# Performance work log

Hardware: AMD Instinct MI355X
Metric: run time of the kernel (lower is better)

The kernel has to match this reference:

```python
import jax, jax.numpy as jnp
import numpy as np

N = 50000        # nodes
E = 1_600_000    # edges (avg degree 32)
D_IN = 128
HID = 256
D_OUT = 128      # must equal D_IN for the residual add


def setup_inputs() -> dict:
    key = jax.random.key(0)
    k0, k1, k2, k3 = jax.random.split(key, 4)
    x = jax.random.normal(k0, (N, D_IN), dtype=jnp.float32)
    edge_index = jax.random.randint(k1, (2, E), 0, N, dtype=jnp.int32)
    # GCNConv params (lin: Linear without bias in PyG, plus additive bias)
    W1 = jax.random.normal(k2, (D_IN, HID), dtype=jnp.float32) / np.sqrt(D_IN)
    b1 = jnp.zeros((HID,), jnp.float32)
    W2 = jax.random.normal(k3, (HID, D_OUT), dtype=jnp.float32) / np.sqrt(HID)
    b2 = jnp.zeros((D_OUT,), jnp.float32)
    return {"x": x, "edge_index": edge_index, "W1": W1, "b1": b1, "W2": W2, "b2": b2}


def _gcn_conv(x, src, dst, norm, W, b, n):
    # PyG GCNConv: transform, gather source features, scale by sym-norm, scatter-add to dst.
    h = x @ W                        # [n, d_out]
    msg = h[src] * norm[:, None]     # [E+n, d_out] gathered messages
    out = jax.ops.segment_sum(msg, dst, num_segments=n)
    return out + b


def reference(x, edge_index, W1, b1, W2, b2):
    n = x.shape[0]
    # add self loops (GCNConv default add_self_loops=True)
    loops = jnp.arange(n, dtype=edge_index.dtype)
    src = jnp.concatenate([edge_index[0], loops])
    dst = jnp.concatenate([edge_index[1], loops])
    # symmetric normalization D^{-1/2} (A+I) D^{-1/2}
    deg = jax.ops.segment_sum(jnp.ones_like(dst, dtype=x.dtype), dst, num_segments=n)
    dinv = jnp.where(deg > 0, jax.lax.rsqrt(deg), 0.0)
    norm = dinv[src] * dinv[dst]
    skip = x  # nn.Identity skip connection
    h = jax.nn.relu(_gcn_conv(x, src, dst, norm, W1, b1, n))
    out = _gcn_conv(h, src, dst, norm, W2, b2, n)
    # classification_layer treated as identity; original .double() cast kept in fp32
    return out + skip
```

## Files before the change

kernel.cpp:

```cpp
#include <hip/hip_runtime.h>

#define D_IN 128
#define HID 256
#define BKT_SHIFT 8
#define BKT_SIZE 256
#define BKT_CAP 10240
#define CHUNK 4096
#define PAD_SLACK 2048
#define LSTR 264
#define ASTR 136

typedef __attribute__((ext_vector_type(8))) short short8;
typedef __attribute__((ext_vector_type(4))) float floatx4;
typedef __attribute__((ext_vector_type(4))) int intx4;

static __device__ __forceinline__ unsigned short f2b(float f) {
  unsigned u = __float_as_uint(f);
  unsigned r = (u + 0x7fffu + ((u >> 16) & 1u)) >> 16;
  return (unsigned short)r;
}

static __device__ __forceinline__ void unpack8(uint4 v, float* f) {
  f[0] = __uint_as_float(v.x << 16); f[1] = __uint_as_float(v.x & 0xffff0000u);
  f[2] = __uint_as_float(v.y << 16); f[3] = __uint_as_float(v.y & 0xffff0000u);
  f[4] = __uint_as_float(v.z << 16); f[5] = __uint_as_float(v.z & 0xffff0000u);
  f[6] = __uint_as_float(v.w << 16); f[7] = __uint_as_float(v.w & 0xffff0000u);
}

static __device__ __forceinline__ void acc_fma(float* acc, uint4 v, float w) {
  float g[8];
  unpack8(v, g);
#pragma unroll
  for (int d = 0; d < 8; ++d) acc[d] = fmaf(g[d], w, acc[d]);
}

static __device__ __forceinline__ void gather_row(float* acc, const uint4* __restrict__ Hq,
                                                  const float* __restrict__ dinv,
                                                  const int* __restrict__ csr,
                                                  int2 se, float dv, int lane) {
  intx4 c0 = *(const intx4*)(csr + se.x);
  intx4 c1 = *(const intx4*)(csr + se.x + 4);
  for (int j = se.x; j < se.y; ) {
    const int jn = j + 8;
    const int jp = (jn < se.y) ? jn : se.x;
    intx4 n0 = *(const intx4*)(csr + jp);
    intx4 n1 = *(const intx4*)(csr + jp + 4);
    float w0 = dinv[c0.x] * dv, w1 = dinv[c0.y] * dv;
    float w2 = dinv[c0.z] * dv, w3 = dinv[c0.w] * dv;
    float w4 = dinv[c1.x] * dv, w5 = dinv[c1.y] * dv;
    float w6 = dinv[c1.z] * dv, w7 = dinv[c1.w] * dv;
    uint4 v0 = Hq[(size_t)c0.x * 16 + lane];
    uint4 v1 = Hq[(size_t)c0.y * 16 + lane];
    uint4 v2 = Hq[(size_t)c0.z * 16 + lane];
    uint4 v3 = Hq[(size_t)c0.w * 16 + lane];
    uint4 v4 = Hq[(size_t)c1.x * 16 + lane];
    uint4 v5 = Hq[(size_t)c1.y * 16 + lane];
    uint4 v6 = Hq[(size_t)c1.z * 16 + lane];
    uint4 v7 = Hq[(size_t)c1.w * 16 + lane];
    acc_fma(acc, v0, w0);
    acc_fma(acc, v1, w1);
    acc_fma(acc, v2, w2);
    acc_fma(acc, v3, w3);
    acc_fma(acc, v4, w4);
    acc_fma(acc, v5, w5);
    acc_fma(acc, v6, w6);
    acc_fma(acc, v7, w7);
    c0 = n0; c1 = n1; j = jn;
  }
}


__global__ __launch_bounds__(256) void fused_front_kernel(
    const int* __restrict__ src, const int* __restrict__ dst,
    int* __restrict__ bkt_cursor, int* __restrict__ ebuf, int E, int nbkt, int nchunk,
    const float4* __restrict__ x4, unsigned short* __restrict__ xb, int n4,
    const float* __restrict__ W1, unsigned short* __restrict__ Wt1,
    const float* __restrict__ W2, unsigned short* __restrict__ Wt2,
    float* __restrict__ dinv, unsigned short* __restrict__ tb, int N) {
  const int bid = blockIdx.x;
  const int tid = threadIdx.x;
  if (bid < nchunk) {
    __shared__ int hist[BKT_SIZE];
    __shared__ int bbase[BKT_SIZE];
    if (tid < nbkt) hist[tid] = 0;
    __syncthreads();
    const int base = bid * CHUNK;
    const int end = min(base + CHUNK, E);
    for (int e = base + tid; e < end; e += 256)
      atomicAdd(&hist[dst[e] >> BKT_SHIFT], 1);
    __syncthreads();
    if (tid < nbkt) {
      int c = hist[tid];
      bbase[tid] = c > 0 ? atomicAdd(&bkt_cursor[tid], c) : 0;
      hist[tid] = 0;
    }
    __syncthreads();
    for (int e = base + tid; e < end; e += 256) {
      int d = dst[e];
      int b = d >> BKT_SHIFT;
      int off = atomicAdd(&hist[b], 1);
      int rel = bbase[b] + off;
      if (rel < BKT_CAP)
        ebuf[b * BKT_CAP + rel] = (src[e] << BKT_SHIFT) | (d & (BKT_SIZE - 1));
    }
    return;
  }
  const int nxblk = (n4 + 255) / 256;
  if (bid < nchunk + nxblk) {
    int i = (bid - nchunk) * 256 + tid;
    if (i >= n4) return;
    float4 v = x4[i];
    ushort4 o;
    o.x = f2b(v.x); o.y = f2b(v.y); o.z = f2b(v.z); o.w = f2b(v.w);
    *(ushort4*)(xb + (size_t)i * 4) = o;
  } else if (bid < nchunk + nxblk + 128) {
    int e = (bid - nchunk - nxblk) * 256 + tid;
    int k = e >> 8, n = e & 255;
    Wt1[(size_t)n * D_IN + k] = f2b(W1[e]);
  } else if (bid < nchunk + nxblk + 256) {
    int e = (bid - nchunk - nxblk - 128) * 256 + tid;
    int k = e >> 7, n = e & 127;
    Wt2[(size_t)n * HID + k] = f2b(W2[e]);
  } else {
    if (tid == 0) dinv[N] = 0.f;
    if (tid < 64)       ((unsigned*)(xb + (size_t)N * D_IN))[tid]      = 0u;
    else if (tid < 128) ((unsigned*)(tb + (size_t)N * D_IN))[tid - 64] = 0u;
  }
}


__global__ __launch_bounds__(256) void bucket_build_kernel(const int* __restrict__ ebuf,
                                                           const int* __restrict__ bkt_cursor,
                                                           float* __restrict__ dinv,
                                                           int2* __restrict__ rowse,
                                                           int* __restrict__ csr,
                                                           int N, int nbkt) {
  __shared__ int hist[BKT_SIZE];
  __shared__ int srs[BKT_SIZE];
  __shared__ int wsums[4];
  const int b = blockIdx.x;
  const int tid = threadIdx.x;
  const int node0 = b << BKT_SHIFT;
  const int nloc = min(BKT_SIZE, N - node0);
  const int ebeg = b * BKT_CAP;
  const int eend = ebeg + min(bkt_cursor[b], BKT_CAP);

  hist[tid] = 0;
  __syncthreads();
  for (int e = ebeg + tid; e < eend; e += 256)
    atomicAdd(&hist[ebuf[e] & (BKT_SIZE - 1)], 1);
  __syncthreads();

  const int h = hist[tid];
  const int p = (h + 7) & ~7;
  const int lane = tid & 63, wid = tid >> 6;
  int incl = p;
#pragma unroll
  for (int off = 1; off < 64; off <<= 1) {
    int t = __shfl_up(incl, off);
    if (lane >= off) incl += t;
  }
  if (lane == 63) wsums[wid] = incl;
  __syncthreads();
  int wex = 0;
  for (int w = 0; w < wid; ++w) wex += wsums[w];
  const int ex = wex + incl - p;
  const int base = b * (BKT_CAP + PAD_SLACK);
  if (tid < nloc) {
    int st = base + ex;
    dinv[node0 + tid] = rsqrtf((float)(h + 1));
    rowse[node0 + tid] = make_int2(st, st + p);
    srs[tid] = st;
  }
  hist[tid] = 0;
  __syncthreads();

  for (int e = ebeg + tid; e < eend; e += 256) {
    int u = ebuf[e];
    int l = u & (BKT_SIZE - 1);
    int pos = atomicAdd(&hist[l], 1);
    csr[srs[l] + pos] = u >> BKT_SHIFT;
  }
  __syncthreads();
  for (int l = tid; l < nloc; l += 256) {
    int deg = hist[l];
    int pp = (deg + 7) & ~7;
    int s0 = srs[l];
    for (int q = s0 + deg; q < s0 + pp; ++q) csr[q] = N;
  }
}


__global__ __launch_bounds__(512, 4) void agg1_gemm_kernel(
    const uint4* __restrict__ Hq, const int2* __restrict__ rowse,
    const int* __restrict__ csr, const float* __restrict__ dinv,
    const unsigned short* __restrict__ Wt1, const float* __restrict__ b1,
    const unsigned short* __restrict__ Wt2, unsigned short* __restrict__ T, int M) {
  __shared__ unsigned short as_[32][ASTR];
  __shared__ unsigned short hs[32][LSTR];
  const int tid = threadIdx.x;
  const int node0 = blockIdx.x * 32;

  {
    const int glane = tid & 15;
    const int lrow = tid >> 4;
    const int node = node0 + lrow;
    float acc[8] = {0.f, 0.f, 0.f, 0.f, 0.f, 0.f, 0.f, 0.f};
    if (node < M) {
      const float dv = dinv[node];
      uint4 sv = Hq[(size_t)node * 16 + glane];
      float f[8];
      unpack8(sv, f);
      const float ws = dv * dv;
#pragma unroll
      for (int d = 0; d < 8; ++d) acc[d] = f[d] * ws;
      gather_row(acc, Hq, dinv, csr, rowse[node], dv, glane);
    }
    uint4 o;
    o.x = (unsigned)f2b(acc[0]) | ((unsigned)f2b(acc[1]) << 16);
    o.y = (unsigned)f2b(acc[2]) | ((unsigned)f2b(acc[3]) << 16);
    o.z = (unsigned)f2b(acc[4]) | ((unsigned)f2b(acc[5]) << 16);
    o.w = (unsigned)f2b(acc[6]) | ((unsigned)f2b(acc[7]) << 16);
    *(uint4*)&as_[lrow][glane * 8] = o;
  }
  __syncthreads();

  const int wave = tid >> 6;
  const int lane = tid & 63;
  const int quad = lane >> 4;
  const int l16 = lane & 15;

  const short8* bp1 = (const short8*)(Wt1 + (size_t)(wave * 32 + l16) * D_IN + quad * 8);
  floatx4 acc1[2][2];
#pragma unroll
  for (int g = 0; g < 2; ++g)
#pragma unroll
    for (int t = 0; t < 2; ++t) acc1[g][t] = floatx4{0.f, 0.f, 0.f, 0.f};

#pragma unroll
  for (int kt = 0; kt < 4; ++kt) {
    short8 a0 = *(const short8*)&as_[0 * 16 + l16][kt * 32 + quad * 8];
    short8 a1 = *(const short8*)&as_[1 * 16 + l16][kt * 32 + quad * 8];
#pragma unroll
    for (int t = 0; t < 2; ++t) {
      short8 b = bp1[kt * 4 + t * 256];
      acc1[0][t] = __builtin_amdgcn_mfma_f32_16x16x32_bf16(a0, b, acc1[0][t], 0, 0, 0);
      acc1[1][t] = __builtin_amdgcn_mfma_f32_16x16x32_bf16(a1, b, acc1[1][t], 0, 0, 0);
    }
  }
#pragma unroll
  for (int t = 0; t < 2; ++t) {
    const float bv = b1[wave * 32 + t * 16 + l16];
#pragma unroll
    for (int g = 0; g < 2; ++g)
#pragma unroll
      for (int r = 0; r < 4; ++r) {
        float v = acc1[g][t][r] + bv;
        v = v > 0.f ? v : 0.f;
        hs[g * 16 + quad * 4 + r][wave * 32 + t * 16 + l16] = f2b(v);
      }
  }
  __syncthreads();

  const short8* bp2 = (const short8*)(Wt2 + (size_t)(wave * 16 + l16) * HID + quad * 8);
  floatx4 acc2[2];
#pragma unroll
  for (int g = 0; g < 2; ++g) acc2[g] = floatx4{0.f, 0.f, 0.f, 0.f};

#pragma unroll
  for (int kt = 0; kt < 8; ++kt) {
    short8 a0 = *(const short8*)&hs[0 * 16 + l16][kt * 32 + quad * 8];
    short8 a1 = *(const short8*)&hs[1 * 16 + l16][kt * 32 + quad * 8];
    short8 b = bp2[kt * 4];
    acc2[0] = __builtin_amdgcn_mfma_f32_16x16x32_bf16(a0, b, acc2[0], 0, 0, 0);
    acc2[1] = __builtin_amdgcn_mfma_f32_16x16x32_bf16(a1, b, acc2[1], 0, 0, 0);
  }
  __syncthreads();

#pragma unroll
  for (int g = 0; g < 2; ++g)
#pragma unroll
    for (int r = 0; r < 4; ++r)
      hs[g * 16 + quad * 4 + r][wave * 16 + l16] = f2b(acc2[g][r]);
  __syncthreads();

  {
    const int r = tid >> 4;
    const int c = (tid & 15) * 8;
    const int row = node0 + r;
    uint4 v = *(const uint4*)&hs[r][c];
    if (row < M) *(uint4*)&T[(size_t)row * D_IN + c] = v;
  }
}


__global__ __launch_bounds__(256) void agg2_kernel(const uint4* __restrict__ Hq,
                                                   const int2* __restrict__ rowse,
                                                   const int* __restrict__ csr,
                                                   const float* __restrict__ dinv,
                                                   const float* __restrict__ skip,
                                                   const float* __restrict__ bias,
                                                   float* __restrict__ OUT, int n) {
  const int lane = threadIdx.x & 15;
  const int node = blockIdx.x * 16 + (threadIdx.x >> 4);
  if (node >= n) return;

  const float dv = dinv[node];
  float acc[8];
  {
    uint4 sv = Hq[(size_t)node * 16 + lane];
    float f[8];
    unpack8(sv, f);
    const float ws = dv * dv;
#pragma unroll
    for (int d = 0; d < 8; ++d) acc[d] = f[d] * ws;
  }
  gather_row(acc, Hq, dinv, csr, rowse[node], dv, lane);

  const float* sp = skip + (size_t)node * 128 + lane * 8;
  const float* bp = bias + lane * 8;
  float4 s0 = *(const float4*)sp, s1 = *(const float4*)(sp + 4);
  float4 b0 = *(const float4*)bp, b1 = *(const float4*)(bp + 4);
  float* op = OUT + (size_t)node * 128 + lane * 8;
  *(float4*)op = make_float4(acc[0] + s0.x + b0.x, acc[1] + s0.y + b0.y,
                             acc[2] + s0.z + b0.z, acc[3] + s0.w + b0.w);
  *(float4*)(op + 4) = make_float4(acc[4] + s1.x + b1.x, acc[5] + s1.y + b1.y,
                                   acc[6] + s1.z + b1.z, acc[7] + s1.w + b1.w);
}


extern "C" void kernel_launch(void* const* d_in, const int* in_sizes, int n_in,
                              void* d_out, int out_size, void* d_ws, size_t ws_size,
                              hipStream_t stream) {
  const float* x  = (const float*)d_in[0];
  const int*   ei = (const int*)d_in[1];
  const float* W1 = (const float*)d_in[2];
  const float* b1 = (const float*)d_in[3];
  const float* W2 = (const float*)d_in[4];
  const float* b2 = (const float*)d_in[5];
  float* out = (float*)d_out;

  const int N = in_sizes[0] / D_IN;
  const int E = in_sizes[1] / 2;
  const int* srcA = ei;
  const int* dstA = ei + E;
  const int NBKT = (N + BKT_SIZE - 1) >> BKT_SHIFT;
  const int NCHUNK = (E + CHUNK - 1) / CHUNK;

  char* ws = (char*)d_ws;
  size_t off = 0;
  auto alloc = [&](size_t bytes) { void* p = ws + off; off = (off + bytes + 255) & ~(size_t)255; return p; };
  int*            bkt_cursor = (int*)           alloc((size_t)NBKT * 4);
  float*          dinv       = (float*)         alloc((size_t)(N + 1) * 4);
  int2*           rowse      = (int2*)          alloc((size_t)N * 8);
  int*            ebuf       = (int*)           alloc((size_t)NBKT * BKT_CAP * 4);
  int*            csr        = (int*)           alloc((size_t)NBKT * (BKT_CAP + PAD_SLACK) * 4);
  unsigned short* xb         = (unsigned short*)alloc((size_t)(N + 1) * D_IN * 2);
  unsigned short* tb         = (unsigned short*)alloc((size_t)(N + 1) * D_IN * 2);
  unsigned short* Wt1        = (unsigned short*)alloc((size_t)D_IN * HID * 2);
  unsigned short* Wt2        = (unsigned short*)alloc((size_t)D_IN * HID * 2);

  const int n4 = N * D_IN / 4;
  const int nxblk = (n4 + 255) / 256;

  (void)hipMemsetAsync(bkt_cursor, 0, (size_t)NBKT * 4, stream);
  fused_front_kernel<<<NCHUNK + nxblk + 256 + 1, 256, 0, stream>>>(
      srcA, dstA, bkt_cursor, ebuf, E, NBKT, NCHUNK,
      (const float4*)x, xb, n4, W1, Wt1, W2, Wt2, dinv, tb, N);
  bucket_build_kernel<<<NBKT, 256, 0, stream>>>(ebuf, bkt_cursor, dinv, rowse, csr, N, NBKT);
  agg1_gemm_kernel<<<(N + 31) / 32, 512, 0, stream>>>((const uint4*)xb, rowse, csr, dinv,
                                                      Wt1, b1, Wt2, tb, N);
  agg2_kernel<<<(N + 15) / 16, 256, 0, stream>>>((const uint4*)tb, rowse, csr,
                                                 dinv, x, b2, out, N);
}
```

Measured before the change: 265.9 us.

## Merge all stages into one persistent cooperative kernel with grid syncs

Replaces the memset plus four separate kernel launches with a single cooperative persistent kernel. It uses grid-stride loops over virtual blocks and grid-wide syncs between the phases: bucketing, bf16 conversion, CSR build, aggregation+GEMM and final aggregation. The aim is to remove launch overhead and inter-kernel gaps. In exchange, the grid is capped by occupancy at 512 threads, the later phases lose the extra parallelism of the old larger launches, and the grid barriers add their own cost.

```diff
diff --git a/kernel.cpp b/kernel.cpp
--- a/kernel.cpp
+++ b/kernel.cpp
@@ -1,4 +1,5 @@
 #include <hip/hip_runtime.h>
+#include <hip/hip_cooperative_groups.h>
 
 #define D_IN 128
 #define HID 256
@@ -70,262 +71,250 @@
 }
 
 
-__global__ __launch_bounds__(256) void fused_front_kernel(
+__global__ __launch_bounds__(512) void mega_kernel(
     const int* __restrict__ src, const int* __restrict__ dst,
-    int* __restrict__ bkt_cursor, int* __restrict__ ebuf, int E, int nbkt, int nchunk,
-    const float4* __restrict__ x4, unsigned short* __restrict__ xb, int n4,
+    int* __restrict__ bkt_cursor, int* __restrict__ ebuf,
+    const float4* __restrict__ x4, unsigned short* __restrict__ xb,
     const float* __restrict__ W1, unsigned short* __restrict__ Wt1,
     const float* __restrict__ W2, unsigned short* __restrict__ Wt2,
-    float* __restrict__ dinv, unsigned short* __restrict__ tb, int N) {
-  const int bid = blockIdx.x;
-  const int tid = threadIdx.x;
-  if (bid < nchunk) {
-    __shared__ int hist[BKT_SIZE];
-    __shared__ int bbase[BKT_SIZE];
-    if (tid < nbkt) hist[tid] = 0;
-    __syncthreads();
-    const int base = bid * CHUNK;
+    float* __restrict__ dinv, int2* __restrict__ rowse, int* __restrict__ csr,
+    const float* __restrict__ b1v, unsigned short* __restrict__ tb,
+    const float* __restrict__ xskip, const float* __restrict__ b2v,
+    float* __restrict__ out,
+    int E, int N, int nbkt, int nchunk, int n4) {
+  namespace cg = cooperative_groups;
+  cg::grid_group gg = cg::this_grid();
+
+  __shared__ union {
+    struct { int hist[BKT_SIZE]; int bbase[BKT_SIZE]; } p1;
+    struct { int hist[BKT_SIZE]; int srs[BKT_SIZE]; int wsums[4]; } p2;
+    struct { unsigned short a[32][ASTR]; unsigned short h[32][LSTR]; } p3;
+  } sm;
+
+  const int bid = blockIdx.x, tid = threadIdx.x;
+  const int gdim = gridDim.x;
+  const int gtid = bid * 512 + tid;
+  const int gstr = gdim * 512;
+
+  for (int i = gtid; i < nbkt; i += gstr) bkt_cursor[i] = 0;
+  gg.sync();
+
+  for (int vb = bid; vb < nchunk; vb += gdim) {
+    if (tid < nbkt) sm.p1.hist[tid] = 0;
+    __syncthreads();
+    const int base = vb * CHUNK;
     const int end = min(base + CHUNK, E);
-    for (int e = base + tid; e < end; e += 256)
-      atomicAdd(&hist[dst[e] >> BKT_SHIFT], 1);
+    for (int e = base + tid; e < end; e += 512)
+      atomicAdd(&sm.p1.hist[dst[e] >> BKT_SHIFT], 1);
     __syncthreads();
     if (tid < nbkt) {
-      int c = hist[tid];
-      bbase[tid] = c > 0 ? atomicAdd(&bkt_cursor[tid], c) : 0;
-      hist[tid] = 0;
-    }
-    __syncthreads();
-    for (int e = base + tid; e < end; e += 256) {
+      int c = sm.p1.hist[tid];
+      sm.p1.bbase[tid] = c > 0 ? atomicAdd(&bkt_cursor[tid], c) : 0;
+      sm.p1.hist[tid] = 0;
+    }
+    __syncthreads();
+    for (int e = base + tid; e < end; e += 512) {
       int d = dst[e];
       int b = d >> BKT_SHIFT;
-      int off = atomicAdd(&hist[b], 1);
-      int rel = bbase[b] + off;
+      int off = atomicAdd(&sm.p1.hist[b], 1);
+      int rel = sm.p1.bbase[b] + off;
       if (rel < BKT_CAP)
         ebuf[b * BKT_CAP + rel] = (src[e] << BKT_SHIFT) | (d & (BKT_SIZE - 1));
     }
-    return;
-  }
-  const int nxblk = (n4 + 255) / 256;
-  if (bid < nchunk + nxblk) {
-    int i = (bid - nchunk) * 256 + tid;
-    if (i >= n4) return;
+    __syncthreads();
+  }
+  for (int i = gtid; i < n4; i += gstr) {
     float4 v = x4[i];
     ushort4 o;
     o.x = f2b(v.x); o.y = f2b(v.y); o.z = f2b(v.z); o.w = f2b(v.w);
     *(ushort4*)(xb + (size_t)i * 4) = o;
-  } else if (bid < nchunk + nxblk + 128) {
-    int e = (bid - nchunk - nxblk) * 256 + tid;
-    int k = e >> 8, n = e & 255;
-    Wt1[(size_t)n * D_IN + k] = f2b(W1[e]);
-  } else if (bid < nchunk + nxblk + 256) {
-    int e = (bid - nchunk - nxblk - 128) * 256 + tid;
-    int k = e >> 7, n = e & 127;
-    Wt2[(size_t)n * HID + k] = f2b(W2[e]);
-  } else {
-    if (tid == 0) dinv[N] = 0.f;
-    if (tid < 64)       ((unsigned*)(xb + (size_t)N * D_IN))[tid]      = 0u;
-    else if (tid < 128) ((unsigned*)(tb + (size_t)N * D_IN))[tid - 64] = 0u;
-  }
-}
-
-
-__global__ __launch_bounds__(256) void bucket_build_kernel(const int* __restrict__ ebuf,
-                                                           const int* __restrict__ bkt_cursor,
-                                                           float* __restrict__ dinv,
-                                                           int2* __restrict__ rowse,
-                                                           int* __restrict__ csr,
-                                                           int N, int nbkt) {
-  __shared__ int hist[BKT_SIZE];
-  __shared__ int srs[BKT_SIZE];
-  __shared__ int wsums[4];
-  const int b = blockIdx.x;
-  const int tid = threadIdx.x;
-  const int node0 = b << BKT_SHIFT;
-  const int nloc = min(BKT_SIZE, N - node0);
-  const int ebeg = b * BKT_CAP;
-  const int eend = ebeg + min(bkt_cursor[b], BKT_CAP);
-
-  hist[tid] = 0;
-  __syncthreads();
-  for (int e = ebeg + tid; e < eend; e += 256)
-    atomicAdd(&hist[ebuf[e] & (BKT_SIZE - 1)], 1);
-  __syncthreads();
-
-  const int h = hist[tid];
-  const int p = (h + 7) & ~7;
-  const int lane = tid & 63, wid = tid >> 6;
-  int incl = p;
-#pragma unroll
-  for (int off = 1; off < 64; off <<= 1) {
-    int t = __shfl_up(incl, off);
-    if (lane >= off) incl += t;
-  }
-  if (lane == 63) wsums[wid] = incl;
-  __syncthreads();
-  int wex = 0;
-  for (int w = 0; w < wid; ++w) wex += wsums[w];
-  const int ex = wex + incl - p;
-  const int base = b * (BKT_CAP + PAD_SLACK);
-  if (tid < nloc) {
-    int st = base + ex;
-    dinv[node0 + tid] = rsqrtf((float)(h + 1));
-    rowse[node0 + tid] = make_int2(st, st + p);
-    srs[tid] = st;
-  }
-  hist[tid] = 0;
-  __syncthreads();
-
-  for (int e = ebeg + tid; e < eend; e += 256) {
-    int u = ebuf[e];
-    int l = u & (BKT_SIZE - 1);
-    int pos = atomicAdd(&hist[l], 1);
-    csr[srs[l] + pos] = u >> BKT_SHIFT;
-  }
-  __syncthreads();
-  for (int l = tid; l < nloc; l += 256) {
-    int deg = hist[l];
-    int pp = (deg + 7) & ~7;
-    int s0 = srs[l];
-    for (int q = s0 + deg; q < s0 + pp; ++q) csr[q] = N;
-  }
-}
-
-
-__global__ __launch_bounds__(512, 4) void agg1_gemm_kernel(
-    const uint4* __restrict__ Hq, const int2* __restrict__ rowse,
-    const int* __restrict__ csr, const float* __restrict__ dinv,
-    const unsigned short* __restrict__ Wt1, const float* __restrict__ b1,
-    const unsigned short* __restrict__ Wt2, unsigned short* __restrict__ T, int M) {
-  __shared__ unsigned short as_[32][ASTR];
-  __shared__ unsigned short hs[32][LSTR];
-  const int tid = threadIdx.x;
-  const int node0 = blockIdx.x * 32;
+  }
+  for (int e = gtid; e < D_IN * HID; e += gstr)
+    Wt1[(size_t)(e & 255) * D_IN + (e >> 8)] = f2b(W1[e]);
+  for (int e = gtid; e < HID * D_IN; e += gstr)
+    Wt2[(size_t)(e & 127) * HID + (e >> 7)] = f2b(W2[e]);
+  if (gtid == 0) dinv[N] = 0.f;
+  if (gtid < 64)       ((unsigned*)(xb + (size_t)N * D_IN))[gtid]      = 0u;
+  else if (gtid < 128) ((unsigned*)(tb + (size_t)N * D_IN))[gtid - 64] = 0u;
+  gg.sync();
+
+  for (int vb = bid; vb < nbkt; vb += gdim) {
+    const int node0 = vb << BKT_SHIFT;
+    const int nloc = min(BKT_SIZE, N - node0);
+    const int ebeg = vb * BKT_CAP;
+    const int eend = ebeg + min(bkt_cursor[vb], BKT_CAP);
+    if (tid < BKT_SIZE) sm.p2.hist[tid] = 0;
+    __syncthreads();
+    for (int e = ebeg + tid; e < eend; e += 512)
+      atomicAdd(&sm.p2.hist[ebuf[e] & (BKT_SIZE - 1)], 1);
+    __syncthreads();
+    int h = 0, p = 0, incl = 0;
+    const int lane = tid & 63, wid = tid >> 6;
+    if (tid < BKT_SIZE) {
+      h = sm.p2.hist[tid];
+      p = (h + 7) & ~7;
+      incl = p;
+#pragma unroll
+      for (int off = 1; off < 64; off <<= 1) {
+        int t = __shfl_up(incl, off);
+        if (lane >= off) incl += t;
+      }
+      if (lane == 63) sm.p2.wsums[wid] = incl;
+    }
+    __syncthreads();
+    if (tid < nloc) {
+      int wex = 0;
+      for (int w = 0; w < wid; ++w) wex += sm.p2.wsums[w];
+      int ex = wex + incl - p;
+      int st = vb * (BKT_CAP + PAD_SLACK) + ex;
+      dinv[node0 + tid] = rsqrtf((float)(h + 1));
+      rowse[node0 + tid] = make_int2(st, st + p);
+      sm.p2.srs[tid] = st;
+    }
+    if (tid < BKT_SIZE) sm.p2.hist[tid] = 0;
+    __syncthreads();
+    for (int e = ebeg + tid; e < eend; e += 512) {
+      int u = ebuf[e];
+      int l = u & (BKT_SIZE - 1);
+      int pos = atomicAdd(&sm.p2.hist[l], 1);
+      csr[sm.p2.srs[l] + pos] = u >> BKT_SHIFT;
+    }
+    __syncthreads();
+    for (int l = tid; l < nloc; l += 512) {
+      int deg = sm.p2.hist[l];
+      int pp = (deg + 7) & ~7;
+      int s0 = sm.p2.srs[l];
+      for (int q = s0 + deg; q < s0 + pp; ++q) csr[q] = N;
+    }
+    __syncthreads();
+  }
+  gg.sync();
 
   {
-    const int glane = tid & 15;
-    const int lrow = tid >> 4;
-    const int node = node0 + lrow;
-    float acc[8] = {0.f, 0.f, 0.f, 0.f, 0.f, 0.f, 0.f, 0.f};
-    if (node < M) {
+    const uint4* Hq = (const uint4*)xb;
+    const int nvb3 = (N + 31) >> 5;
+    for (int vb = bid; vb < nvb3; vb += gdim) {
+      const int node0 = vb * 32;
+      {
+        const int glane = tid & 15;
+        const int lrow = tid >> 4;
+        const int node = node0 + lrow;
+        float acc[8] = {0.f, 0.f, 0.f, 0.f, 0.f, 0.f, 0.f, 0.f};
+        if (node < N) {
+          const float dv = dinv[node];
+          uint4 sv = Hq[(size_t)node * 16 + glane];
+          float f[8];
+          unpack8(sv, f);
+          const float ws = dv * dv;
+#pragma unroll
+          for (int d = 0; d < 8; ++d) acc[d] = f[d] * ws;
+          gather_row(acc, Hq, dinv, csr, rowse[node], dv, glane);
+        }
+        uint4 o;
+        o.x = (unsigned)f2b(acc[0]) | ((unsigned)f2b(acc[1]) << 16);
+        o.y = (unsigned)f2b(acc[2]) | ((unsigned)f2b(acc[3]) << 16);
+        o.z = (unsigned)f2b(acc[4]) | ((unsigned)f2b(acc[5]) << 16);
+        o.w = (unsigned)f2b(acc[6]) | ((unsigned)f2b(acc[7]) << 16);
+        *(uint4*)&sm.p3.a[lrow][glane * 8] = o;
+      }
+      __syncthreads();
+
+      const int wave = tid >> 6;
+      const int lane = tid & 63;
+      const int quad = lane >> 4;
+      const int l16 = lane & 15;
+
+      const short8* bp1 = (const short8*)(Wt1 + (size_t)(wave * 32 + l16) * D_IN + quad * 8);
+      floatx4 acc1[2][2];
+#pragma unroll
+      for (int g = 0; g < 2; ++g)
+#pragma unroll
+        for (int t = 0; t < 2; ++t) acc1[g][t] = floatx4{0.f, 0.f, 0.f, 0.f};
+#pragma unroll
+      for (int kt = 0; kt < 4; ++kt) {
+        short8 a0 = *(const short8*)&sm.p3.a[0 * 16 + l16][kt * 32 + quad * 8];
+        short8 a1 = *(const short8*)&sm.p3.a[1 * 16 + l16][kt * 32 + quad * 8];
+#pragma unroll
+        for (int t = 0; t < 2; ++t) {
+          short8 b = bp1[kt * 4 + t * 256];
+          acc1[0][t] = __builtin_amdgcn_mfma_f32_16x16x32_bf16(a0, b, acc1[0][t], 0, 0, 0);
+          acc1[1][t] = __builtin_amdgcn_mfma_f32_16x16x32_bf16(a1, b, acc1[1][t], 0, 0, 0);
+        }
+      }
+#pragma unroll
+      for (int t = 0; t < 2; ++t) {
+        const float bv = b1v[wave * 32 + t * 16 + l16];
+#pragma unroll
+        for (int g = 0; g < 2; ++g)
+#pragma unroll
+          for (int r = 0; r < 4; ++r) {
+            float v = acc1[g][t][r] + bv;
+            v = v > 0.f ? v : 0.f;
+            sm.p3.h[g * 16 + quad * 4 + r][wave * 32 + t * 16 + l16] = f2b(v);
+          }
+      }
+      __syncthreads();
+
+      const short8* bp2 = (const short8*)(Wt2 + (size_t)(wave * 16 + l16) * HID + quad * 8);
+      floatx4 acc2[2];
+#pragma unroll
+      for (int g = 0; g < 2; ++g) acc2[g] = floatx4{0.f, 0.f, 0.f, 0.f};
+#pragma unroll
+      for (int kt = 0; kt < 8; ++kt) {
+        short8 a0 = *(const short8*)&sm.p3.h[0 * 16 + l16][kt * 32 + quad * 8];
+        short8 a1 = *(const short8*)&sm.p3.h[1 * 16 + l16][kt * 32 + quad * 8];
+        short8 b = bp2[kt * 4];
+        acc2[0] = __builtin_amdgcn_mfma_f32_16x16x32_bf16(a0, b, acc2[0], 0, 0, 0);
+        acc2[1] = __builtin_amdgcn_mfma_f32_16x16x32_bf16(a1, b, acc2[1], 0, 0, 0);
+      }
+      __syncthreads();
+
+#pragma unroll
+      for (int g = 0; g < 2; ++g)
+#pragma unroll
+        for (int r = 0; r < 4; ++r)
+          sm.p3.h[g * 16 + quad * 4 + r][wave * 16 + l16] = f2b(acc2[g][r]);
+      __syncthreads();
+
+      {
+        const int r = tid >> 4;
+        const int c = (tid & 15) * 8;
+        const int row = node0 + r;
+        uint4 v = *(const uint4*)&sm.p3.h[r][c];
+        if (row < N) *(uint4*)&tb[(size_t)row * D_IN + c] = v;
+      }
+    }
+  }
+  gg.sync();
+
+  {
+    const uint4* Hq = (const uint4*)tb;
+    const int lane = gtid & 15;
+    const int nstep = gstr >> 4;
+    for (int node = gtid >> 4; node < N; node += nstep) {
       const float dv = dinv[node];
-      uint4 sv = Hq[(size_t)node * 16 + glane];
-      float f[8];
-      unpack8(sv, f);
-      const float ws = dv * dv;
-#pragma unroll
-      for (int d = 0; d < 8; ++d) acc[d] = f[d] * ws;
-      gather_row(acc, Hq, dinv, csr, rowse[node], dv, glane);
-    }
-    uint4 o;
-    o.x = (unsigned)f2b(acc[0]) | ((unsigned)f2b(acc[1]) << 16);
-    o.y = (unsigned)f2b(acc[2]) | ((unsigned)f2b(acc[3]) << 16);
-    o.z = (unsigned)f2b(acc[4]) | ((unsigned)f2b(acc[5]) << 16);
-    o.w = (unsigned)f2b(acc[6]) | ((unsigned)f2b(acc[7]) << 16);
-    *(uint4*)&as_[lrow][glane * 8] = o;
-  }
-  __syncthreads();
-
-  const int wave = tid >> 6;
-  const int lane = tid & 63;
-  const int quad = lane >> 4;
-  const int l16 = lane & 15;
-
-  const short8* bp1 = (const short8*)(Wt1 + (size_t)(wave * 32 + l16) * D_IN + quad * 8);
-  floatx4 acc1[2][2];
-#pragma unroll
-  for (int g = 0; g < 2; ++g)
-#pragma unroll
-    for (int t = 0; t < 2; ++t) acc1[g][t] = floatx4{0.f, 0.f, 0.f, 0.f};
-
-#pragma unroll
-  for (int kt = 0; kt < 4; ++kt) {
-    short8 a0 = *(const short8*)&as_[0 * 16 + l16][kt * 32 + quad * 8];
-    short8 a1 = *(const short8*)&as_[1 * 16 + l16][kt * 32 + quad * 8];
-#pragma unroll
-    for (int t = 0; t < 2; ++t) {
-      short8 b = bp1[kt * 4 + t * 256];
-      acc1[0][t] = __builtin_amdgcn_mfma_f32_16x16x32_bf16(a0, b, acc1[0][t], 0, 0, 0);
-      acc1[1][t] = __builtin_amdgcn_mfma_f32_16x16x32_bf16(a1, b, acc1[1][t], 0, 0, 0);
-    }
-  }
-#pragma unroll
-  for (int t = 0; t < 2; ++t) {
-    const float bv = b1[wave * 32 + t * 16 + l16];
-#pragma unroll
-    for (int g = 0; g < 2; ++g)
-#pragma unroll
-      for (int r = 0; r < 4; ++r) {
-        float v = acc1[g][t][r] + bv;
-        v = v > 0.f ? v : 0.f;
-        hs[g * 16 + quad * 4 + r][wave * 32 + t * 16 + l16] = f2b(v);
-      }
-  }
-  __syncthreads();
-
-  const short8* bp2 = (const short8*)(Wt2 + (size_t)(wave * 16 + l16) * HID + quad * 8);
-  floatx4 acc2[2];
-#pragma unroll
-  for (int g = 0; g < 2; ++g) acc2[g] = floatx4{0.f, 0.f, 0.f, 0.f};
-
-#pragma unroll
-  for (int kt = 0; kt < 8; ++kt) {
-    short8 a0 = *(const short8*)&hs[0 * 16 + l16][kt * 32 + quad * 8];
-    short8 a1 = *(const short8*)&hs[1 * 16 + l16][kt * 32 + quad * 8];
-    short8 b = bp2[kt * 4];
-    acc2[0] = __builtin_amdgcn_mfma_f32_16x16x32_bf16(a0, b, acc2[0], 0, 0, 0);
-    acc2[1] = __builtin_amdgcn_mfma_f32_16x16x32_bf16(a1, b, acc2[1], 0, 0, 0);
-  }
-  __syncthreads();
-
-#pragma unroll
-  for (int g = 0; g < 2; ++g)
-#pragma unroll
-    for (int r = 0; r < 4; ++r)
-      hs[g * 16 + quad * 4 + r][wave * 16 + l16] = f2b(acc2[g][r]);
-  __syncthreads();
-
-  {
-    const int r = tid >> 4;
-    const int c = (tid & 15) * 8;
-    const int row = node0 + r;
-    uint4 v = *(const uint4*)&hs[r][c];
-    if (row < M) *(uint4*)&T[(size_t)row * D_IN + c] = v;
-  }
-}
-
-
-__global__ __launch_bounds__(256) void agg2_kernel(const uint4* __restrict__ Hq,
-                                                   const int2* __restrict__ rowse,
-                                                   const int* __restrict__ csr,
-                                                   const float* __restrict__ dinv,
-                                                   const float* __restrict__ skip,
-                                                   const float* __restrict__ bias,
-                                                   float* __restrict__ OUT, int n) {
-  const int lane = threadIdx.x & 15;
-  const int node = blockIdx.x * 16 + (threadIdx.x >> 4);
-  if (node >= n) return;
-
-  const float dv = dinv[node];
-  float acc[8];
-  {
-    uint4 sv = Hq[(size_t)node * 16 + lane];
-    float f[8];
-    unpack8(sv, f);
-    const float ws = dv * dv;
-#pragma unroll
-    for (int d = 0; d < 8; ++d) acc[d] = f[d] * ws;
-  }
-  gather_row(acc, Hq, dinv, csr, rowse[node], dv, lane);
-
-  const float* sp = skip + (size_t)node * 128 + lane * 8;
-  const float* bp = bias + lane * 8;
-  float4 s0 = *(const float4*)sp, s1 = *(const float4*)(sp + 4);
-  float4 b0 = *(const float4*)bp, b1 = *(const float4*)(bp + 4);
-  float* op = OUT + (size_t)node * 128 + lane * 8;
-  *(float4*)op = make_float4(acc[0] + s0.x + b0.x, acc[1] + s0.y + b0.y,
-                             acc[2] + s0.z + b0.z, acc[3] + s0.w + b0.w);
-  *(float4*)(op + 4) = make_float4(acc[4] + s1.x + b1.x, acc[5] + s1.y + b1.y,
-                                   acc[6] + s1.z + b1.z, acc[7] + s1.w + b1.w);
+      float acc[8];
+      {
+        uint4 sv = Hq[(size_t)node * 16 + lane];
+        float f[8];
+        unpack8(sv, f);
+        const float ws = dv * dv;
+#pragma unroll
+        for (int d = 0; d < 8; ++d) acc[d] = f[d] * ws;
+      }
+      gather_row(acc, Hq, dinv, csr, rowse[node], dv, lane);
+
+      const float* sp = xskip + (size_t)node * 128 + lane * 8;
+      const float* bp = b2v + lane * 8;
+      float4 s0 = *(const float4*)sp, s1 = *(const float4*)(sp + 4);
+      float4 b0 = *(const float4*)bp, b1 = *(const float4*)(bp + 4);
+      float* op = out + (size_t)node * 128 + lane * 8;
+      *(float4*)op = make_float4(acc[0] + s0.x + b0.x, acc[1] + s0.y + b0.y,
+                                 acc[2] + s0.z + b0.z, acc[3] + s0.w + b0.w);
+      *(float4*)(op + 4) = make_float4(acc[4] + s1.x + b1.x, acc[5] + s1.y + b1.y,
+                                       acc[6] + s1.z + b1.z, acc[7] + s1.w + b1.w);
+    }
+  }
 }
 
 
@@ -346,6 +335,7 @@
   const int* dstA = ei + E;
   const int NBKT = (N + BKT_SIZE - 1) >> BKT_SHIFT;
   const int NCHUNK = (E + CHUNK - 1) / CHUNK;
+  const int n4 = N * D_IN / 4;
 
   char* ws = (char*)d_ws;
   size_t off = 0;
@@ -360,16 +350,29 @@
   unsigned short* Wt1        = (unsigned short*)alloc((size_t)D_IN * HID * 2);
   unsigned short* Wt2        = (unsigned short*)alloc((size_t)D_IN * HID * 2);
 
-  const int n4 = N * D_IN / 4;
-  const int nxblk = (n4 + 255) / 256;
-
-  (void)hipMemsetAsync(bkt_cursor, 0, (size_t)NBKT * 4, stream);
-  fused_front_kernel<<<NCHUNK + nxblk + 256 + 1, 256, 0, stream>>>(
-      srcA, dstA, bkt_cursor, ebuf, E, NBKT, NCHUNK,
-      (const float4*)x, xb, n4, W1, Wt1, W2, Wt2, dinv, tb, N);
-  bucket_build_kernel<<<NBKT, 256, 0, stream>>>(ebuf, bkt_cursor, dinv, rowse, csr, N, NBKT);
-  agg1_gemm_kernel<<<(N + 31) / 32, 512, 0, stream>>>((const uint4*)xb, rowse, csr, dinv,
-                                                      Wt1, b1, Wt2, tb, N);
-  agg2_kernel<<<(N + 15) / 16, 256, 0, stream>>>((const uint4*)tb, rowse, csr,
-                                                 dinv, x, b2, out, N);
-}
+  static int coopGrid = 0;
+  if (coopGrid == 0) {
+    int dev = 0;
+    (void)hipGetDevice(&dev);
+    hipDeviceProp_t prop;
+    (void)hipGetDeviceProperties(&prop, dev);
+    int nb = 0;
+    (void)hipOccupancyMaxActiveBlocksPerMultiprocessor(&nb, mega_kernel, 512, 0);
+    if (nb < 1) nb = 1;
+    coopGrid = nb * prop.multiProcessorCount;
+    if (coopGrid < 1) coopGrid = 256;
+  }
+  int grid = coopGrid;
+  const int maxwork = (N + 31) / 32;
+  if (grid > maxwork) grid = maxwork;
+
+  const float4* x4 = (const float4*)x;
+  void* args[] = {
+      (void*)&srcA, (void*)&dstA, (void*)&bkt_cursor, (void*)&ebuf,
+      (void*)&x4, (void*)&xb, (void*)&W1, (void*)&Wt1, (void*)&W2, (void*)&Wt2,
+      (void*)&dinv, (void*)&rowse, (void*)&csr, (void*)&b1, (void*)&tb,
+      (void*)&x, (void*)&b2, (void*)&out,
+      (void*)&E, (void*)&N, (void*)&NBKT, (void*)&NCHUNK, (void*)&n4};
+  (void)hipLaunchCooperativeKernel((void*)mega_kernel, dim3(grid), dim3(512),
+                                   args, 0, stream);
+}
```

Measured after the change: 399.5 us. 1.5x slower.
